# Kernel tuning notes

Measured on AMD Instinct MI355X. Metric: run time of the kernel, lower is better.

## Reference

```python
import jax, jax.numpy as jnp
import numpy as np

H = 1024  # latent_dim / GRU hidden size


def setup_inputs() -> dict:
    key = jax.random.key(0)
    ks = jax.random.split(key, 7)
    B, T, E, V = 16, 256, 512, 32000
    return {
        "latent_samples": jax.random.normal(ks[0], (B, H), jnp.float32),
        "true_outputs": jax.random.normal(ks[1], (B, T, E), jnp.float32),
        "gru_kernel": jax.random.normal(ks[2], (E, 3 * H), jnp.float32) * 0.02,
        "gru_rec_kernel": jax.random.normal(ks[3], (H, 3 * H), jnp.float32) * 0.02,
        "gru_bias": jax.random.normal(ks[4], (2, 3 * H), jnp.float32) * 0.02,
        "dense_w": jax.random.normal(ks[5], (H, V), jnp.float32) * 0.02,
        "dense_b": jax.random.normal(ks[6], (V,), jnp.float32) * 0.02,
    }


def reference(latent_samples, true_outputs, gru_kernel, gru_rec_kernel, gru_bias, dense_w, dense_b):
    # teacher_forcing_decode: GRU over true_outputs[:, :-1, :] with initial state latent_samples,
    # then TimeDistributed Dense to vocab logits. Keras GRU, reset_after=True, gate order z|r|h.
    teacher = true_outputs[:, :-1, :]                      # [B, T-1, E]
    # Precompute all input projections at once: [B, T-1, 3H]
    x_proj = jnp.einsum('bte,eg->btg', teacher, gru_kernel) + gru_bias[0]
    rec_bias = gru_bias[1]

    def step(h, x_t):  # h: [B,H], x_t: [B,3H]
        rec = h @ gru_rec_kernel + rec_bias              # [B,3H]
        xz, xr, xh = jnp.split(x_t, 3, axis=-1)
        rz, rr, rh = jnp.split(rec, 3, axis=-1)
        z = jax.nn.sigmoid(xz + rz)
        r = jax.nn.sigmoid(xr + rr)
        hh = jnp.tanh(xh + r * rh)
        h_new = z * h + (1.0 - z) * hh
        return h_new, h_new

    _, hs = jax.lax.scan(step, latent_samples, jnp.swapaxes(x_proj, 0, 1))  # hs: [T-1, B, H]
    gru_out = jnp.swapaxes(hs, 0, 1)                       # [B, T-1, H]
    logits = jnp.einsum('bth,hv->btv', gru_out, dense_w) + dense_b
    return logits
```

## Files before the change

### kernel.cpp

```cpp
#include <hip/hip_runtime.h>


typedef __attribute__((ext_vector_type(8))) short s16x8;
typedef __attribute__((ext_vector_type(4))) float f32x4;
typedef __attribute__((ext_vector_type(4))) int   i32x4;

#define B_      16
#define TSTEPS  255
#define H_      1024
#define G_      3072
#define E_      512
#define V_      32000
#define MROWS   4080
#define MPAD    4096
#define NBLK_SCAN 64
#define NWORK     448
#define NBLK_TOT  512
#define NTILE_RB  32
#define NTILE_CB  250
#define FSTRIDE   16
#define PROG_IDX  1024

__device__ __forceinline__ short f2bf(float f) {
  unsigned u = __float_as_uint(f);
  u = (u + 0x7fffu + ((u >> 16) & 1u)) >> 16;
  return (short)u;
}

__device__ __forceinline__ float frcp(float x) {
  float r;
  asm("v_rcp_f32 %0, %1" : "=v"(r) : "v"(x));
  return r;
}

__device__ __forceinline__ i32x4 ld16_sc(const void* p) {
  i32x4 v;
  asm volatile("global_load_dwordx4 %0, %1, off sc0 sc1" : "=v"(v) : "v"(p) : "memory");
  return v;
}

__device__ __forceinline__ void gload_lds16(const short* g, void* l) {
  __builtin_amdgcn_global_load_lds((const __attribute__((address_space(1))) void*)g,
                                   (__attribute__((address_space(3))) void*)l,
                                   16, 0, 0);
}


__global__ void transpose_cvt(const float* __restrict__ src, short* __restrict__ dst,
                              int K, int N) {
  __shared__ float tile[32][33];
  const int n0 = blockIdx.x * 32, k0 = blockIdx.y * 32;
  const int tx = threadIdx.x, ty0 = threadIdx.y;
#pragma unroll
  for (int yy = 0; yy < 4; ++yy) {
    int ty = ty0 + yy * 8;
    tile[ty][tx] = src[(size_t)(k0 + ty) * N + (n0 + tx)];
  }
  __syncthreads();
#pragma unroll
  for (int yy = 0; yy < 4; ++yy) {
    int ty = ty0 + yy * 8;
    dst[(size_t)(n0 + ty) * K + (k0 + tx)] = f2bf(tile[tx][ty]);
  }
}

__global__ void pack_teacher(const float* __restrict__ src, short* __restrict__ dst) {
  int idx = blockIdx.x * 256 + threadIdx.x;
  int row = idx >> 6;
  int c8 = (idx & 63) << 3;
  int t = row >> 4, b = row & 15;
  s16x8 v = {};
  if (t < TSTEPS) {
    const float* s = src + ((size_t)(b * 256 + t)) * E_ + c8;
#pragma unroll
    for (int j = 0; j < 8; ++j) v[j] = f2bf(s[j]);
  }
  *(s16x8*)(dst + (size_t)row * E_ + c8) = v;
}

__global__ void init_h(const float* __restrict__ latent, short* __restrict__ hbuf) {
  int i = blockIdx.x * 256 + threadIdx.x;
  hbuf[i] = f2bf(latent[i]);
}

__global__ __launch_bounds__(256) void gemm_bf16(
    const short* __restrict__ A, const short* __restrict__ BT,
    const float* __restrict__ bias, float* __restrict__ C, int N, int K) {
  const int tid = threadIdx.x;
  const int lane = tid & 63, w = tid >> 6;
  const int r = lane & 15, q = lane >> 4;
  const int bm = blockIdx.y * 128, bn = blockIdx.x * 128;
  const int wm = bm + (w >> 1) * 64, wn = bn + (w & 1) * 64;
  const short* Ab = A + (size_t)(wm + r) * K + q * 8;
  const short* Bb = BT + (size_t)(wn + r) * K + q * 8;
  f32x4 acc[4][4] = {};
  s16x8 a0[4], b0[4], a1[4], b1[4];
  const int nk = K >> 5;
#define GL(AA, BB, kk)                                                         \
  {                                                                            \
    _Pragma("unroll") for (int i = 0; i < 4; ++i) {                            \
      AA[i] = *(const s16x8*)(Ab + (size_t)i * 16 * K + (kk) * 32);            \
    }                                                                          \
    _Pragma("unroll") for (int j = 0; j < 4; ++j) {                            \
      BB[j] = *(const s16x8*)(Bb + (size_t)j * 16 * K + (kk) * 32);            \
    }                                                                          \
  }
#define MM(AA, BB)                                                             \
  {                                                                            \
    _Pragma("unroll") for (int i = 0; i < 4; ++i)                              \
        _Pragma("unroll") for (int j = 0; j < 4; ++j)                          \
            acc[i][j] = __builtin_amdgcn_mfma_f32_16x16x32_bf16(               \
                AA[i], BB[j], acc[i][j], 0, 0, 0);                             \
  }
  GL(a0, b0, 0)
#pragma unroll 1
  for (int ks = 0; ks < nk; ks += 2) {
    GL(a1, b1, ks + 1)
    MM(a0, b0)
    if (ks + 2 < nk) GL(a0, b0, ks + 2)
    MM(a1, b1)
  }
#undef GL
#undef MM
#pragma unroll
  for (int j = 0; j < 4; ++j) {
    const int col = wn + j * 16 + r;
    const float bv = bias[col];
#pragma unroll
    for (int i = 0; i < 4; ++i) {
#pragma unroll
      for (int rr = 0; rr < 4; ++rr) {
        const int row = wm + i * 16 + q * 4 + rr;
        C[(size_t)row * N + col] = acc[i][j][rr] + bv;
      }
    }
  }
}

__global__ __launch_bounds__(256, 2) void fused_scan_gemm(
    const short* __restrict__ WrecT,
    const float* __restrict__ xproj,
    const float* __restrict__ bias1,
    const float* __restrict__ latent,
    short* __restrict__ hbuf,
    short* __restrict__ gruout,
    const short* __restrict__ DwT,
    const float* __restrict__ db,
    float* __restrict__ out,
    unsigned* __restrict__ sync) {
  const int tid = threadIdx.x, lane = tid & 63, w = tid >> 6;
  const int r = lane & 15, q = lane >> 4;
  __shared__ s16x8 smem_v[2048];

  if (blockIdx.x < NBLK_SCAN) {
    __builtin_amdgcn_s_setprio(3);
    float (*red)[3][64][4] = (float(*)[3][64][4])smem_v;
    const int c = blockIdx.x;
    s16x8 wb[3][8];
#pragma unroll
    for (int g = 0; g < 3; ++g)
#pragma unroll
      for (int s = 0; s < 8; ++s)
        wb[g][s] = *(const s16x8*)(WrecT + (size_t)(g * 1024 + c * 16 + r) * 1024 +
                                   (w * 8 + s) * 32 + q * 8);

    const int m = tid >> 4, nl = tid & 15, col = c * 16 + nl;
    float h = latent[m * 1024 + col];
    const float bz = bias1[col], brr = bias1[1024 + col], bhh = bias1[2048 + col];
    const float* xb = xproj + (size_t)m * G_;
    short* hb0 = hbuf;
    short* hb1 = hbuf + 16 * 1024;
    float xz = xb[col], xr = xb[1024 + col], xh = xb[2048 + col];

    for (int t = 0; t < TSTEPS; ++t) {
      const short* hcur = (t & 1) ? hb1 : hb0;
      short* hnxt = (t & 1) ? hb0 : hb1;
      i32x4 afi[8];
#pragma unroll
      for (int s = 0; s < 8; ++s)
        afi[s] = ld16_sc(hcur + r * 1024 + (w * 8 + s) * 32 + q * 8);
      asm volatile("s_waitcnt vmcnt(0)"
                   : "+v"(afi[0]), "+v"(afi[1]), "+v"(afi[2]), "+v"(afi[3]),
                     "+v"(afi[4]), "+v"(afi[5]), "+v"(afi[6]), "+v"(afi[7])
                   :: "memory");
      __builtin_amdgcn_sched_barrier(0);
      f32x4 acc[3] = {};
#pragma unroll
      for (int s = 0; s < 8; ++s) {
        const s16x8 af = *(const s16x8*)&afi[s];
        acc[0] = __builtin_amdgcn_mfma_f32_16x16x32_bf16(af, wb[0][s], acc[0], 0, 0, 0);
        acc[1] = __builtin_amdgcn_mfma_f32_16x16x32_bf16(af, wb[1][s], acc[1], 0, 0, 0);
        acc[2] = __builtin_amdgcn_mfma_f32_16x16x32_bf16(af, wb[2][s], acc[2], 0, 0, 0);
      }
      *(f32x4*)&red[w][0][lane][0] = acc[0];
      *(f32x4*)&red[w][1][lane][0] = acc[1];
      *(f32x4*)&red[w][2][lane][0] = acc[2];
      __syncthreads();
      const int rl = (m >> 2) * 16 + nl, ri = m & 3;
      float rz = bz, rr2 = brr, rh = bhh;
#pragma unroll
      for (int ww = 0; ww < 4; ++ww) {
        rz += red[ww][0][rl][ri];
        rr2 += red[ww][1][rl][ri];
        rh += red[ww][2][rl][ri];
      }
      const float z = frcp(1.f + __expf(-(xz + rz)));
      const float rg = frcp(1.f + __expf(-(xr + rr2)));
      const float hh = tanhf(xh + rg * rh);
      h = z * h + (1.f - z) * hh;
      const unsigned hb = (unsigned short)f2bf(h);
      const unsigned nb = __shfl(hb, lane | 1, 64);
      const unsigned pv = hb | (nb << 16);
      if (!(tid & 1))
        __hip_atomic_store((unsigned*)hnxt + ((m * 1024 + col) >> 1), pv,
                           __ATOMIC_RELAXED, __HIP_MEMORY_SCOPE_AGENT);
      __syncthreads();
      if (tid == 0)
        __hip_atomic_store(&sync[c * FSTRIDE], (unsigned)(t + 1),
                           __ATOMIC_RELAXED, __HIP_MEMORY_SCOPE_AGENT);
      if (!(tid & 1))
        __hip_atomic_store((unsigned*)gruout + (((size_t)(t * 16 + m)) * 1024 + col) / 2,
                           pv, __ATOMIC_RELAXED, __HIP_MEMORY_SCOPE_AGENT);
      {
        const float* xn = xb + (size_t)(t + 1) * 16 * G_;
        xz = xn[col]; xr = xn[1024 + col]; xh = xn[2048 + col];
      }
      if (t < TSTEPS - 1) {
        const int fl = lane;
        unsigned v = __hip_atomic_load(&sync[fl * FSTRIDE], __ATOMIC_RELAXED,
                                       __HIP_MEMORY_SCOPE_AGENT);
        while (!__all(v > (unsigned)t)) {
          __builtin_amdgcn_s_sleep(1);
          v = __hip_atomic_load(&sync[fl * FSTRIDE], __ATOMIC_RELAXED,
                                __HIP_MEMORY_SCOPE_AGENT);
        }
        if (c == 0 && tid == 0)
          __hip_atomic_store(&sync[PROG_IDX], (unsigned)(t + 1),
                             __ATOMIC_RELAXED, __HIP_MEMORY_SCOPE_AGENT);
      }
    }
    asm volatile("s_waitcnt vmcnt(0)" ::: "memory");
    __syncthreads();
    if (tid == 0)
      __hip_atomic_store(&sync[c * FSTRIDE], 256u,
                         __ATOMIC_RELAXED, __HIP_MEMORY_SCOPE_AGENT);
    if (c == 0) {
      unsigned v = __hip_atomic_load(&sync[lane * FSTRIDE], __ATOMIC_RELAXED,
                                     __HIP_MEMORY_SCOPE_AGENT);
      while (!__all(v >= 256u)) {
        __builtin_amdgcn_s_sleep(1);
        v = __hip_atomic_load(&sync[lane * FSTRIDE], __ATOMIC_RELAXED,
                              __HIP_MEMORY_SCOPE_AGENT);
      }
      if (tid == 0)
        __hip_atomic_store(&sync[PROG_IDX], 256u,
                           __ATOMIC_RELAXED, __HIP_MEMORY_SCOPE_AGENT);
    }
  } else {
    char* sb = (char*)smem_v;
    const int wr = w >> 1, wc = w & 1;
    const int j = blockIdx.x - NBLK_SCAN;
#pragma unroll 1
    for (int tq = j; tq < NTILE_RB * NTILE_CB; tq += NWORK) {
      const int rb = tq / NTILE_CB, cb = tq - rb * NTILE_CB;
      const unsigned need = (unsigned)(min(254, rb * 8 + 7) + 2);
      unsigned pv = __hip_atomic_load(&sync[PROG_IDX], __ATOMIC_RELAXED,
                                      __HIP_MEMORY_SCOPE_AGENT);
      while (pv < need) {
        __builtin_amdgcn_s_sleep(32);
        pv = __hip_atomic_load(&sync[PROG_IDX], __ATOMIC_RELAXED,
                               __HIP_MEMORY_SCOPE_AGENT);
      }
      const short* Ag = gruout + (size_t)rb * 128 * 1024;
      const short* Bg = DwT + (size_t)cb * 128 * 1024;
      f32x4 acc[4][4] = {};
#define STAGE(buf, kk)                                                         \
  {                                                                            \
    _Pragma("unroll") for (int it = 0; it < 2; ++it) {                         \
      const size_t go = (size_t)(w * 32 + it * 16 + (lane >> 2)) * 1024 +      \
                        (kk) * 32 + (lane & 3) * 8;                            \
      char* lb = sb + (buf) * 16384 + w * 2048 + it * 1024;                    \
      gload_lds16(Ag + go, lb);                                                \
      gload_lds16(Bg + go, lb + 8192);                                         \
    }                                                                          \
  }
      STAGE(0, 0)
#pragma unroll 1
      for (int kk = 0; kk < 32; ++kk) {
        __syncthreads();
        if (kk < 31) STAGE((kk + 1) & 1, kk + 1)
        const char* ab = sb + (kk & 1) * 16384;
        s16x8 af[4], bf[4];
#pragma unroll
        for (int i = 0; i < 4; ++i)
          af[i] = *(const s16x8*)(ab + (wr * 64 + i * 16 + r) * 64 + q * 16);
#pragma unroll
        for (int j5 = 0; j5 < 4; ++j5)
          bf[j5] = *(const s16x8*)(ab + 8192 + (wc * 64 + j5 * 16 + r) * 64 + q * 16);
#pragma unroll
        for (int i = 0; i < 4; ++i)
#pragma unroll
          for (int j5 = 0; j5 < 4; ++j5)
            acc[i][j5] = __builtin_amdgcn_mfma_f32_16x16x32_bf16(
                af[i], bf[j5], acc[i][j5], 0, 0, 0);
      }
#undef STAGE
      const int wm = rb * 128 + wr * 64, wn = cb * 128 + wc * 64;
#pragma unroll
      for (int j2 = 0; j2 < 4; ++j2) {
        const int col = wn + j2 * 16 + r;
        const float bv = db[col];
#pragma unroll
        for (int i = 0; i < 4; ++i) {
#pragma unroll
          for (int rr = 0; rr < 4; ++rr) {
            const int arow = wm + i * 16 + q * 4 + rr;
            const int t = arow >> 4, mm = arow & 15;
            if (t < TSTEPS)
              __builtin_nontemporal_store(
                  acc[i][j2][rr] + bv,
                  &out[(size_t)(mm * TSTEPS + t) * V_ + col]);
          }
        }
      }
      __syncthreads();
    }
  }
}

extern "C" void kernel_launch(void* const* d_in, const int* in_sizes, int n_in,
                              void* d_out, int out_size, void* d_ws, size_t ws_size,
                              hipStream_t stream) {
  const float* latent = (const float*)d_in[0];
  const float* trueo  = (const float*)d_in[1];
  const float* gk     = (const float*)d_in[2];
  const float* grk    = (const float*)d_in[3];
  const float* gbias  = (const float*)d_in[4];
  const float* dw     = (const float*)d_in[5];
  const float* db     = (const float*)d_in[6];
  float* out = (float*)d_out;
  char* ws = (char*)d_ws;
  short*    WrecT  = (short*)(ws + 0);
  short*    GkT    = (short*)(ws + 6291456);
  short*    DwT    = (short*)(ws + 9437184);
  short*    teachA = (short*)(ws + 74973184);
  float*    xproj  = (float*)(ws + 79167488);
  short*    gruout = (short*)(ws + 129499136);
  short*    hbuf   = (short*)(ws + 137887744);
  unsigned* syncb  = (unsigned*)(ws + 137953280);

  hipMemsetAsync(syncb, 0, 8192, stream);
  transpose_cvt<<<dim3(96, 32), dim3(32, 8), 0, stream>>>(grk, WrecT, 1024, 3072);
  transpose_cvt<<<dim3(96, 16), dim3(32, 8), 0, stream>>>(gk, GkT, 512, 3072);
  transpose_cvt<<<dim3(1000, 32), dim3(32, 8), 0, stream>>>(dw, DwT, 1024, 32000);
  pack_teacher<<<1024, 256, 0, stream>>>(trueo, teachA);
  init_h<<<64, 256, 0, stream>>>(latent, hbuf);
  gemm_bf16<<<dim3(24, 32), 256, 0, stream>>>(teachA, GkT, gbias, xproj, G_, E_);
  fused_scan_gemm<<<NBLK_TOT, 256, 0, stream>>>(WrecT, xproj, gbias + G_, latent,
                                                hbuf, gruout, DwT, db, out, syncb);
}
```

Measured before the change: 971.3 us.

## Replace per-step scan barrier with tagged fp32 hidden state polling

The scan blocks no longer wait on a global all-block flag barrier every step. Each block instead stores the hidden state as fp32 with a 2-bit step tag in the low mantissa bits, and consumers spin-read the hidden vector until every tag matches the expected step. The cost removed is the per-step cross-block barrier round trip. Progress flags are now published only every 8 steps, and the dense GEMM workers poll the per-block flags directly instead of an aggregated progress index. The change also double-buffers the LDS reduction area and adds an XOR swizzle to the GEMM LDS layout to reduce bank conflicts, at the cost of twice the h read bandwidth, small precision loss from the tag bits, and reuse of the teacher buffer region for hbuf.

```diff
diff --git a/kernel.cpp b/kernel.cpp
--- a/kernel.cpp
+++ b/kernel.cpp
@@ -19,7 +19,6 @@
 #define NTILE_RB  32
 #define NTILE_CB  250
 #define FSTRIDE   16
-#define PROG_IDX  1024
 
 __device__ __forceinline__ short f2bf(float f) {
   unsigned u = __float_as_uint(f);
@@ -33,11 +32,15 @@
   return r;
 }
 
-__device__ __forceinline__ i32x4 ld16_sc(const void* p) {
-  i32x4 v;
-  asm volatile("global_load_dwordx4 %0, %1, off sc0 sc1" : "=v"(v) : "v"(p) : "memory");
-  return v;
-}
+__device__ __forceinline__ unsigned cvtpk(float lo, float hi) {
+  unsigned r;
+  asm("v_cvt_pk_bf16_f32 %0, %1, %2" : "=v"(r) : "v"(lo), "v"(hi));
+  return r;
+}
+
+#define GLD_SC(dst, p)                                                         \
+  asm volatile("global_load_dwordx4 %0, %1, off sc0 sc1"                       \
+               : "=v"(dst) : "v"(p) : "memory")
 
 __device__ __forceinline__ void gload_lds16(const short* g, void* l) {
   __builtin_amdgcn_global_load_lds((const __attribute__((address_space(1))) void*)g,
@@ -78,9 +81,11 @@
   *(s16x8*)(dst + (size_t)row * E_ + c8) = v;
 }
 
-__global__ void init_h(const float* __restrict__ latent, short* __restrict__ hbuf) {
+__global__ void init_h(const float* __restrict__ latent, float* __restrict__ hb) {
   int i = blockIdx.x * 256 + threadIdx.x;
-  hbuf[i] = f2bf(latent[i]);
+  unsigned u = __float_as_uint(latent[i]) & ~3u;
+  ((unsigned*)hb)[i] = u;
+  ((unsigned*)hb)[16384 + i] = 3u;
 }
 
 __global__ __launch_bounds__(256) void gemm_bf16(
@@ -141,8 +146,7 @@
     const short* __restrict__ WrecT,
     const float* __restrict__ xproj,
     const float* __restrict__ bias1,
-    const float* __restrict__ latent,
-    short* __restrict__ hbuf,
+    float* __restrict__ hbuf,
     short* __restrict__ gruout,
     const short* __restrict__ DwT,
     const float* __restrict__ db,
@@ -154,7 +158,8 @@
 
   if (blockIdx.x < NBLK_SCAN) {
     __builtin_amdgcn_s_setprio(3);
-    float (*red)[3][64][4] = (float(*)[3][64][4])smem_v;
+    typedef float RedT[4][3][64][4];
+    RedT* red = (RedT*)smem_v;
     const int c = blockIdx.x;
     s16x8 wb[3][8];
 #pragma unroll
@@ -165,78 +170,92 @@
                                    (w * 8 + s) * 32 + q * 8);
 
     const int m = tid >> 4, nl = tid & 15, col = c * 16 + nl;
-    float h = latent[m * 1024 + col];
     const float bz = bias1[col], brr = bias1[1024 + col], bhh = bias1[2048 + col];
     const float* xb = xproj + (size_t)m * G_;
-    short* hb0 = hbuf;
-    short* hb1 = hbuf + 16 * 1024;
+    float* hb0 = hbuf;
+    float* hb1 = hbuf + 16 * 1024;
+    float h = 0.f;
+    {
+      h = hb0[m * 1024 + col];
+    }
     float xz = xb[col], xr = xb[1024 + col], xh = xb[2048 + col];
 
     for (int t = 0; t < TSTEPS; ++t) {
-      const short* hcur = (t & 1) ? hb1 : hb0;
-      short* hnxt = (t & 1) ? hb0 : hb1;
-      i32x4 afi[8];
-#pragma unroll
-      for (int s = 0; s < 8; ++s)
-        afi[s] = ld16_sc(hcur + r * 1024 + (w * 8 + s) * 32 + q * 8);
-      asm volatile("s_waitcnt vmcnt(0)"
-                   : "+v"(afi[0]), "+v"(afi[1]), "+v"(afi[2]), "+v"(afi[3]),
-                     "+v"(afi[4]), "+v"(afi[5]), "+v"(afi[6]), "+v"(afi[7])
-                   :: "memory");
-      __builtin_amdgcn_sched_barrier(0);
+      const float* hcur = (t & 1) ? hb1 : hb0;
+      float* hnxt = (t & 1) ? hb0 : hb1;
+      const int tg = (t >> 1) & 3;
+      const float* lb = hcur + r * 1024 + w * 256 + q * 8;
+      i32x4 va[16];
+      for (;;) {
+#pragma unroll
+        for (int s = 0; s < 8; ++s) {
+          GLD_SC(va[2 * s], lb + s * 32);
+          GLD_SC(va[2 * s + 1], lb + s * 32 + 4);
+        }
+        asm volatile("s_waitcnt vmcnt(0)" ::: "memory");
+        __builtin_amdgcn_sched_barrier(0);
+        unsigned bad = 0;
+#pragma unroll
+        for (int k2 = 0; k2 < 16; ++k2) {
+          bad |= (unsigned)(va[k2][0] ^ tg) | (unsigned)(va[k2][1] ^ tg) |
+                 (unsigned)(va[k2][2] ^ tg) | (unsigned)(va[k2][3] ^ tg);
+        }
+        if (__all((bad & 3u) == 0u)) break;
+        __builtin_amdgcn_s_sleep(1);
+      }
+      s16x8 af[8];
+#pragma unroll
+      for (int s = 0; s < 8; ++s) {
+        union { unsigned u[4]; s16x8 v; } pk;
+        pk.u[0] = cvtpk(__int_as_float(va[2*s][0]), __int_as_float(va[2*s][1]));
+        pk.u[1] = cvtpk(__int_as_float(va[2*s][2]), __int_as_float(va[2*s][3]));
+        pk.u[2] = cvtpk(__int_as_float(va[2*s+1][0]), __int_as_float(va[2*s+1][1]));
+        pk.u[3] = cvtpk(__int_as_float(va[2*s+1][2]), __int_as_float(va[2*s+1][3]));
+        af[s] = pk.v;
+      }
       f32x4 acc[3] = {};
 #pragma unroll
       for (int s = 0; s < 8; ++s) {
-        const s16x8 af = *(const s16x8*)&afi[s];
-        acc[0] = __builtin_amdgcn_mfma_f32_16x16x32_bf16(af, wb[0][s], acc[0], 0, 0, 0);
-        acc[1] = __builtin_amdgcn_mfma_f32_16x16x32_bf16(af, wb[1][s], acc[1], 0, 0, 0);
-        acc[2] = __builtin_amdgcn_mfma_f32_16x16x32_bf16(af, wb[2][s], acc[2], 0, 0, 0);
-      }
-      *(f32x4*)&red[w][0][lane][0] = acc[0];
-      *(f32x4*)&red[w][1][lane][0] = acc[1];
-      *(f32x4*)&red[w][2][lane][0] = acc[2];
+        acc[0] = __builtin_amdgcn_mfma_f32_16x16x32_bf16(af[s], wb[0][s], acc[0], 0, 0, 0);
+        acc[1] = __builtin_amdgcn_mfma_f32_16x16x32_bf16(af[s], wb[1][s], acc[1], 0, 0, 0);
+        acc[2] = __builtin_amdgcn_mfma_f32_16x16x32_bf16(af[s], wb[2][s], acc[2], 0, 0, 0);
+      }
+      *(f32x4*)&red[t & 1][w][0][lane][0] = acc[0];
+      *(f32x4*)&red[t & 1][w][1][lane][0] = acc[1];
+      *(f32x4*)&red[t & 1][w][2][lane][0] = acc[2];
       __syncthreads();
       const int rl = (m >> 2) * 16 + nl, ri = m & 3;
       float rz = bz, rr2 = brr, rh = bhh;
 #pragma unroll
       for (int ww = 0; ww < 4; ++ww) {
-        rz += red[ww][0][rl][ri];
-        rr2 += red[ww][1][rl][ri];
-        rh += red[ww][2][rl][ri];
+        rz += red[t & 1][ww][0][rl][ri];
+        rr2 += red[t & 1][ww][1][rl][ri];
+        rh += red[t & 1][ww][2][rl][ri];
       }
       const float z = frcp(1.f + __expf(-(xz + rz)));
       const float rg = frcp(1.f + __expf(-(xr + rr2)));
       const float hh = tanhf(xh + rg * rh);
       h = z * h + (1.f - z) * hh;
-      const unsigned hb = (unsigned short)f2bf(h);
-      const unsigned nb = __shfl(hb, lane | 1, 64);
-      const unsigned pv = hb | (nb << 16);
-      if (!(tid & 1))
-        __hip_atomic_store((unsigned*)hnxt + ((m * 1024 + col) >> 1), pv,
-                           __ATOMIC_RELAXED, __HIP_MEMORY_SCOPE_AGENT);
-      __syncthreads();
-      if (tid == 0)
-        __hip_atomic_store(&sync[c * FSTRIDE], (unsigned)(t + 1),
-                           __ATOMIC_RELAXED, __HIP_MEMORY_SCOPE_AGENT);
+      const unsigned ntg = (unsigned)(((t + 1) >> 1) & 3);
+      const unsigned hu = (__float_as_uint(h) & ~3u) | ntg;
+      __hip_atomic_store((unsigned*)hnxt + (m * 1024 + col), hu,
+                         __ATOMIC_RELAXED, __HIP_MEMORY_SCOPE_AGENT);
+      const unsigned hb16 = (unsigned short)f2bf(h);
+      const unsigned nb = __shfl(hb16, lane | 1, 64);
+      const unsigned pv = hb16 | (nb << 16);
       if (!(tid & 1))
         __hip_atomic_store((unsigned*)gruout + (((size_t)(t * 16 + m)) * 1024 + col) / 2,
                            pv, __ATOMIC_RELAXED, __HIP_MEMORY_SCOPE_AGENT);
+      if ((t & 7) == 7) {
+        asm volatile("s_waitcnt vmcnt(0)" ::: "memory");
+        __syncthreads();
+        if (tid == 0)
+          __hip_atomic_store(&sync[c * FSTRIDE], (unsigned)(t + 1),
+                             __ATOMIC_RELAXED, __HIP_MEMORY_SCOPE_AGENT);
+      }
       {
         const float* xn = xb + (size_t)(t + 1) * 16 * G_;
         xz = xn[col]; xr = xn[1024 + col]; xh = xn[2048 + col];
-      }
-      if (t < TSTEPS - 1) {
-        const int fl = lane;
-        unsigned v = __hip_atomic_load(&sync[fl * FSTRIDE], __ATOMIC_RELAXED,
-                                       __HIP_MEMORY_SCOPE_AGENT);
-        while (!__all(v > (unsigned)t)) {
-          __builtin_amdgcn_s_sleep(1);
-          v = __hip_atomic_load(&sync[fl * FSTRIDE], __ATOMIC_RELAXED,
-                                __HIP_MEMORY_SCOPE_AGENT);
-        }
-        if (c == 0 && tid == 0)
-          __hip_atomic_store(&sync[PROG_IDX], (unsigned)(t + 1),
-                             __ATOMIC_RELAXED, __HIP_MEMORY_SCOPE_AGENT);
       }
     }
     asm volatile("s_waitcnt vmcnt(0)" ::: "memory");
@@ -244,32 +263,22 @@
     if (tid == 0)
       __hip_atomic_store(&sync[c * FSTRIDE], 256u,
                          __ATOMIC_RELAXED, __HIP_MEMORY_SCOPE_AGENT);
-    if (c == 0) {
-      unsigned v = __hip_atomic_load(&sync[lane * FSTRIDE], __ATOMIC_RELAXED,
-                                     __HIP_MEMORY_SCOPE_AGENT);
-      while (!__all(v >= 256u)) {
-        __builtin_amdgcn_s_sleep(1);
-        v = __hip_atomic_load(&sync[lane * FSTRIDE], __ATOMIC_RELAXED,
-                              __HIP_MEMORY_SCOPE_AGENT);
-      }
-      if (tid == 0)
-        __hip_atomic_store(&sync[PROG_IDX], 256u,
-                           __ATOMIC_RELAXED, __HIP_MEMORY_SCOPE_AGENT);
-    }
   } else {
     char* sb = (char*)smem_v;
     const int wr = w >> 1, wc = w & 1;
+    const int xterm = ((q ^ ((r >> 1) & 3)) << 4);
+    const int swz8 = (((lane & 3) ^ ((lane >> 3) & 3)) << 3);
     const int j = blockIdx.x - NBLK_SCAN;
 #pragma unroll 1
     for (int tq = j; tq < NTILE_RB * NTILE_CB; tq += NWORK) {
       const int rb = tq / NTILE_CB, cb = tq - rb * NTILE_CB;
-      const unsigned need = (unsigned)(min(254, rb * 8 + 7) + 2);
-      unsigned pv = __hip_atomic_load(&sync[PROG_IDX], __ATOMIC_RELAXED,
-                                      __HIP_MEMORY_SCOPE_AGENT);
-      while (pv < need) {
+      const unsigned need = (unsigned)(rb < 31 ? 8 * rb + 8 : 256);
+      unsigned v = __hip_atomic_load(&sync[lane * FSTRIDE], __ATOMIC_RELAXED,
+                                     __HIP_MEMORY_SCOPE_AGENT);
+      while (!__all(v >= need)) {
         __builtin_amdgcn_s_sleep(32);
-        pv = __hip_atomic_load(&sync[PROG_IDX], __ATOMIC_RELAXED,
-                               __HIP_MEMORY_SCOPE_AGENT);
+        v = __hip_atomic_load(&sync[lane * FSTRIDE], __ATOMIC_RELAXED,
+                              __HIP_MEMORY_SCOPE_AGENT);
       }
       const short* Ag = gruout + (size_t)rb * 128 * 1024;
       const short* Bg = DwT + (size_t)cb * 128 * 1024;
@@ -278,10 +287,10 @@
   {                                                                            \
     _Pragma("unroll") for (int it = 0; it < 2; ++it) {                         \
       const size_t go = (size_t)(w * 32 + it * 16 + (lane >> 2)) * 1024 +      \
-                        (kk) * 32 + (lane & 3) * 8;                            \
-      char* lb = sb + (buf) * 16384 + w * 2048 + it * 1024;                    \
-      gload_lds16(Ag + go, lb);                                                \
-      gload_lds16(Bg + go, lb + 8192);                                         \
+                        (kk) * 32 + swz8;                                      \
+      char* lb2 = sb + (buf) * 16384 + w * 2048 + it * 1024;                   \
+      gload_lds16(Ag + go, lb2);                                               \
+      gload_lds16(Bg + go, lb2 + 8192);                                        \
     }                                                                          \
   }
       STAGE(0, 0)
@@ -293,10 +302,10 @@
         s16x8 af[4], bf[4];
 #pragma unroll
         for (int i = 0; i < 4; ++i)
-          af[i] = *(const s16x8*)(ab + (wr * 64 + i * 16 + r) * 64 + q * 16);
+          af[i] = *(const s16x8*)(ab + (wr * 64 + i * 16 + r) * 64 + xterm);
 #pragma unroll
         for (int j5 = 0; j5 < 4; ++j5)
-          bf[j5] = *(const s16x8*)(ab + 8192 + (wc * 64 + j5 * 16 + r) * 64 + q * 16);
+          bf[j5] = *(const s16x8*)(ab + 8192 + (wc * 64 + j5 * 16 + r) * 64 + xterm);
 #pragma unroll
         for (int i = 0; i < 4; ++i)
 #pragma unroll
@@ -344,9 +353,9 @@
   short*    GkT    = (short*)(ws + 6291456);
   short*    DwT    = (short*)(ws + 9437184);
   short*    teachA = (short*)(ws + 74973184);
+  float*    hbuf   = (float*)(ws + 74973184);
   float*    xproj  = (float*)(ws + 79167488);
   short*    gruout = (short*)(ws + 129499136);
-  short*    hbuf   = (short*)(ws + 137887744);
   unsigned* syncb  = (unsigned*)(ws + 137953280);
 
   hipMemsetAsync(syncb, 0, 8192, stream);
@@ -354,8 +363,8 @@
   transpose_cvt<<<dim3(96, 16), dim3(32, 8), 0, stream>>>(gk, GkT, 512, 3072);
   transpose_cvt<<<dim3(1000, 32), dim3(32, 8), 0, stream>>>(dw, DwT, 1024, 32000);
   pack_teacher<<<1024, 256, 0, stream>>>(trueo, teachA);
+  gemm_bf16<<<dim3(24, 32), 256, 0, stream>>>(teachA, GkT, gbias, xproj, G_, E_);
   init_h<<<64, 256, 0, stream>>>(latent, hbuf);
-  gemm_bf16<<<dim3(24, 32), 256, 0, stream>>>(teachA, GkT, gbias, xproj, G_, E_);
-  fused_scan_gemm<<<NBLK_TOT, 256, 0, stream>>>(WrecT, xproj, gbias + G_, latent,
-                                                hbuf, gruout, DwT, db, out, syncb);
-}
+  fused_scan_gemm<<<NBLK_TOT, 256, 0, stream>>>(WrecT, xproj, gbias + G_, hbuf,
+                                                gruout, DwT, db, out, syncb);
+}
```

Measured after the change: 1.247 ms. 1.28x slower.

## Replicate hidden state and flags, per-block frontiers, swizzle LDS in logits GEMM

Applied to the files above, without the earlier changes.

The scan blocks now write the hidden state and their step flags into eight replicated copies, and each block reads its own copy (chosen by block index mod 8). This is meant to cut contention on the shared lines the 64 scan blocks poll each step. The old single progress counter, advanced by block 0, is replaced by per-block frontier flags published every 8 steps, which the GEMM workers check directly, and the sleep in the scan spin loop is removed. The logits GEMM also gets an XOR swizzle on its LDS tiles to avoid bank conflicts. In exchange the scan does more global stores per step, the frontier lags by up to 8 steps, and the workspace is reorganised so hbuf and the flags reuse the teacher buffer after the projection GEMM.

```diff
diff --git a/kernel.cpp b/kernel.cpp
--- a/kernel.cpp
+++ b/kernel.cpp
@@ -19,7 +19,8 @@
 #define NTILE_RB  32
 #define NTILE_CB  250
 #define FSTRIDE   16
-#define PROG_IDX  1024
+#define NCOPY     8
+#define HCPY      16384
 
 __device__ __forceinline__ short f2bf(float f) {
   unsigned u = __float_as_uint(f);
@@ -33,11 +34,9 @@
   return r;
 }
 
-__device__ __forceinline__ i32x4 ld16_sc(const void* p) {
-  i32x4 v;
-  asm volatile("global_load_dwordx4 %0, %1, off sc0 sc1" : "=v"(v) : "v"(p) : "memory");
-  return v;
-}
+#define GLD_SC(dst, p)                                                         \
+  asm volatile("global_load_dwordx4 %0, %1, off sc0 sc1"                       \
+               : "=v"(dst) : "v"(p) : "memory")
 
 __device__ __forceinline__ void gload_lds16(const short* g, void* l) {
   __builtin_amdgcn_global_load_lds((const __attribute__((address_space(1))) void*)g,
@@ -78,9 +77,11 @@
   *(s16x8*)(dst + (size_t)row * E_ + c8) = v;
 }
 
-__global__ void init_h(const float* __restrict__ latent, short* __restrict__ hbuf) {
+__global__ void init_h(const float* __restrict__ latent, short* __restrict__ hb) {
   int i = blockIdx.x * 256 + threadIdx.x;
-  hbuf[i] = f2bf(latent[i]);
+  const short v = f2bf(latent[i]);
+#pragma unroll
+  for (int cp = 0; cp < NCOPY; ++cp) hb[cp * HCPY + i] = v;
 }
 
 __global__ __launch_bounds__(256) void gemm_bf16(
@@ -151,11 +152,14 @@
   const int tid = threadIdx.x, lane = tid & 63, w = tid >> 6;
   const int r = lane & 15, q = lane >> 4;
   __shared__ s16x8 smem_v[2048];
+  unsigned* scanflag = sync;
+  unsigned* frontier = sync + NCOPY * 1024;
 
   if (blockIdx.x < NBLK_SCAN) {
     __builtin_amdgcn_s_setprio(3);
     float (*red)[3][64][4] = (float(*)[3][64][4])smem_v;
     const int c = blockIdx.x;
+    const int cp = c & 7;
     s16x8 wb[3][8];
 #pragma unroll
     for (int g = 0; g < 3; ++g)
@@ -168,17 +172,15 @@
     float h = latent[m * 1024 + col];
     const float bz = bias1[col], brr = bias1[1024 + col], bhh = bias1[2048 + col];
     const float* xb = xproj + (size_t)m * G_;
-    short* hb0 = hbuf;
-    short* hb1 = hbuf + 16 * 1024;
     float xz = xb[col], xr = xb[1024 + col], xh = xb[2048 + col];
 
     for (int t = 0; t < TSTEPS; ++t) {
-      const short* hcur = (t & 1) ? hb1 : hb0;
-      short* hnxt = (t & 1) ? hb0 : hb1;
+      const short* hcur = hbuf + ((size_t)((t & 1) * NCOPY + cp)) * HCPY;
+      unsigned* hnxt = (unsigned*)(hbuf + (size_t)((t & 1) ^ 1) * NCOPY * HCPY);
       i32x4 afi[8];
 #pragma unroll
       for (int s = 0; s < 8; ++s)
-        afi[s] = ld16_sc(hcur + r * 1024 + (w * 8 + s) * 32 + q * 8);
+        GLD_SC(afi[s], hcur + r * 1024 + (w * 8 + s) * 32 + q * 8);
       asm volatile("s_waitcnt vmcnt(0)"
                    : "+v"(afi[0]), "+v"(afi[1]), "+v"(afi[2]), "+v"(afi[3]),
                      "+v"(afi[4]), "+v"(afi[5]), "+v"(afi[6]), "+v"(afi[7])
@@ -208,68 +210,66 @@
       const float rg = frcp(1.f + __expf(-(xr + rr2)));
       const float hh = tanhf(xh + rg * rh);
       h = z * h + (1.f - z) * hh;
-      const unsigned hb = (unsigned short)f2bf(h);
-      const unsigned nb = __shfl(hb, lane | 1, 64);
-      const unsigned pv = hb | (nb << 16);
-      if (!(tid & 1))
-        __hip_atomic_store((unsigned*)hnxt + ((m * 1024 + col) >> 1), pv,
-                           __ATOMIC_RELAXED, __HIP_MEMORY_SCOPE_AGENT);
+      const unsigned hb16 = (unsigned short)f2bf(h);
+      const unsigned nb = __shfl(hb16, lane | 1, 64);
+      const unsigned pv = hb16 | (nb << 16);
+      const unsigned hoff = (unsigned)((m * 1024 + col) >> 1);
+      if (!(tid & 1)) {
+#pragma unroll
+        for (int cp2 = 0; cp2 < NCOPY; ++cp2)
+          __hip_atomic_store(hnxt + cp2 * (HCPY / 2) + hoff, pv,
+                             __ATOMIC_RELAXED, __HIP_MEMORY_SCOPE_AGENT);
+      }
       __syncthreads();
-      if (tid == 0)
-        __hip_atomic_store(&sync[c * FSTRIDE], (unsigned)(t + 1),
-                           __ATOMIC_RELAXED, __HIP_MEMORY_SCOPE_AGENT);
+      if (tid == 0) {
+#pragma unroll
+        for (int cp2 = 0; cp2 < NCOPY; ++cp2)
+          __hip_atomic_store(&scanflag[cp2 * 1024 + c * FSTRIDE], (unsigned)(t + 1),
+                             __ATOMIC_RELAXED, __HIP_MEMORY_SCOPE_AGENT);
+      }
       if (!(tid & 1))
         __hip_atomic_store((unsigned*)gruout + (((size_t)(t * 16 + m)) * 1024 + col) / 2,
                            pv, __ATOMIC_RELAXED, __HIP_MEMORY_SCOPE_AGENT);
+      if ((t & 7) == 7) {
+        asm volatile("s_waitcnt vmcnt(0)" ::: "memory");
+        __syncthreads();
+        if (tid == 0)
+          __hip_atomic_store(&frontier[c * FSTRIDE], (unsigned)(t + 1),
+                             __ATOMIC_RELAXED, __HIP_MEMORY_SCOPE_AGENT);
+      }
       {
         const float* xn = xb + (size_t)(t + 1) * 16 * G_;
         xz = xn[col]; xr = xn[1024 + col]; xh = xn[2048 + col];
       }
       if (t < TSTEPS - 1) {
-        const int fl = lane;
-        unsigned v = __hip_atomic_load(&sync[fl * FSTRIDE], __ATOMIC_RELAXED,
+        const unsigned* fp = &scanflag[cp * 1024 + lane * FSTRIDE];
+        unsigned v = __hip_atomic_load(fp, __ATOMIC_RELAXED,
                                        __HIP_MEMORY_SCOPE_AGENT);
-        while (!__all(v > (unsigned)t)) {
-          __builtin_amdgcn_s_sleep(1);
-          v = __hip_atomic_load(&sync[fl * FSTRIDE], __ATOMIC_RELAXED,
-                                __HIP_MEMORY_SCOPE_AGENT);
-        }
-        if (c == 0 && tid == 0)
-          __hip_atomic_store(&sync[PROG_IDX], (unsigned)(t + 1),
-                             __ATOMIC_RELAXED, __HIP_MEMORY_SCOPE_AGENT);
+        while (!__all(v > (unsigned)t))
+          v = __hip_atomic_load(fp, __ATOMIC_RELAXED, __HIP_MEMORY_SCOPE_AGENT);
       }
     }
     asm volatile("s_waitcnt vmcnt(0)" ::: "memory");
     __syncthreads();
     if (tid == 0)
-      __hip_atomic_store(&sync[c * FSTRIDE], 256u,
+      __hip_atomic_store(&frontier[c * FSTRIDE], 256u,
                          __ATOMIC_RELAXED, __HIP_MEMORY_SCOPE_AGENT);
-    if (c == 0) {
-      unsigned v = __hip_atomic_load(&sync[lane * FSTRIDE], __ATOMIC_RELAXED,
-                                     __HIP_MEMORY_SCOPE_AGENT);
-      while (!__all(v >= 256u)) {
-        __builtin_amdgcn_s_sleep(1);
-        v = __hip_atomic_load(&sync[lane * FSTRIDE], __ATOMIC_RELAXED,
-                              __HIP_MEMORY_SCOPE_AGENT);
-      }
-      if (tid == 0)
-        __hip_atomic_store(&sync[PROG_IDX], 256u,
-                           __ATOMIC_RELAXED, __HIP_MEMORY_SCOPE_AGENT);
-    }
   } else {
     char* sb = (char*)smem_v;
     const int wr = w >> 1, wc = w & 1;
+    const int xterm = ((q ^ ((r >> 1) & 3)) << 4);
+    const int swz8 = (((lane & 3) ^ ((lane >> 3) & 3)) << 3);
     const int j = blockIdx.x - NBLK_SCAN;
 #pragma unroll 1
     for (int tq = j; tq < NTILE_RB * NTILE_CB; tq += NWORK) {
       const int rb = tq / NTILE_CB, cb = tq - rb * NTILE_CB;
-      const unsigned need = (unsigned)(min(254, rb * 8 + 7) + 2);
-      unsigned pv = __hip_atomic_load(&sync[PROG_IDX], __ATOMIC_RELAXED,
-                                      __HIP_MEMORY_SCOPE_AGENT);
-      while (pv < need) {
+      const unsigned need = (unsigned)(rb < 31 ? 8 * rb + 8 : 256);
+      unsigned v = __hip_atomic_load(&frontier[lane * FSTRIDE], __ATOMIC_RELAXED,
+                                     __HIP_MEMORY_SCOPE_AGENT);
+      while (!__all(v >= need)) {
         __builtin_amdgcn_s_sleep(32);
-        pv = __hip_atomic_load(&sync[PROG_IDX], __ATOMIC_RELAXED,
-                               __HIP_MEMORY_SCOPE_AGENT);
+        v = __hip_atomic_load(&frontier[lane * FSTRIDE], __ATOMIC_RELAXED,
+                              __HIP_MEMORY_SCOPE_AGENT);
       }
       const short* Ag = gruout + (size_t)rb * 128 * 1024;
       const short* Bg = DwT + (size_t)cb * 128 * 1024;
@@ -278,10 +278,10 @@
   {                                                                            \
     _Pragma("unroll") for (int it = 0; it < 2; ++it) {                         \
       const size_t go = (size_t)(w * 32 + it * 16 + (lane >> 2)) * 1024 +      \
-                        (kk) * 32 + (lane & 3) * 8;                            \
-      char* lb = sb + (buf) * 16384 + w * 2048 + it * 1024;                    \
-      gload_lds16(Ag + go, lb);                                                \
-      gload_lds16(Bg + go, lb + 8192);                                         \
+                        (kk) * 32 + swz8;                                      \
+      char* lb2 = sb + (buf) * 16384 + w * 2048 + it * 1024;                   \
+      gload_lds16(Ag + go, lb2);                                               \
+      gload_lds16(Bg + go, lb2 + 8192);                                        \
     }                                                                          \
   }
       STAGE(0, 0)
@@ -293,10 +293,10 @@
         s16x8 af[4], bf[4];
 #pragma unroll
         for (int i = 0; i < 4; ++i)
-          af[i] = *(const s16x8*)(ab + (wr * 64 + i * 16 + r) * 64 + q * 16);
+          af[i] = *(const s16x8*)(ab + (wr * 64 + i * 16 + r) * 64 + xterm);
 #pragma unroll
         for (int j5 = 0; j5 < 4; ++j5)
-          bf[j5] = *(const s16x8*)(ab + 8192 + (wc * 64 + j5 * 16 + r) * 64 + q * 16);
+          bf[j5] = *(const s16x8*)(ab + 8192 + (wc * 64 + j5 * 16 + r) * 64 + xterm);
 #pragma unroll
         for (int i = 0; i < 4; ++i)
 #pragma unroll
@@ -344,18 +344,18 @@
   short*    GkT    = (short*)(ws + 6291456);
   short*    DwT    = (short*)(ws + 9437184);
   short*    teachA = (short*)(ws + 74973184);
+  short*    hbuf   = (short*)(ws + 74973184);
+  unsigned* syncb  = (unsigned*)(ws + 75497472);
   float*    xproj  = (float*)(ws + 79167488);
   short*    gruout = (short*)(ws + 129499136);
-  short*    hbuf   = (short*)(ws + 137887744);
-  unsigned* syncb  = (unsigned*)(ws + 137953280);
-
-  hipMemsetAsync(syncb, 0, 8192, stream);
+
   transpose_cvt<<<dim3(96, 32), dim3(32, 8), 0, stream>>>(grk, WrecT, 1024, 3072);
   transpose_cvt<<<dim3(96, 16), dim3(32, 8), 0, stream>>>(gk, GkT, 512, 3072);
   transpose_cvt<<<dim3(1000, 32), dim3(32, 8), 0, stream>>>(dw, DwT, 1024, 32000);
   pack_teacher<<<1024, 256, 0, stream>>>(trueo, teachA);
+  gemm_bf16<<<dim3(24, 32), 256, 0, stream>>>(teachA, GkT, gbias, xproj, G_, E_);
+  hipMemsetAsync(syncb, 0, 36864, stream);
   init_h<<<64, 256, 0, stream>>>(latent, hbuf);
-  gemm_bf16<<<dim3(24, 32), 256, 0, stream>>>(teachA, GkT, gbias, xproj, G_, E_);
   fused_scan_gemm<<<NBLK_TOT, 256, 0, stream>>>(WrecT, xproj, gbias + G_, latent,
                                                 hbuf, gruout, DwT, db, out, syncb);
 }
```

After: 980.3 us. Within noise of the previous version (+0.9%).
